# Performance work log

Measured on AMD Instinct MI355X. Metric: run time of the kernel, lower is better.

The kernel has to match this reference:

```python
import jax, jax.numpy as jnp
import numpy as np

N, C, H, W = 8, 256, 28, 28
K = 64
EPS = 1e-12  # F.normalize eps
BN_EPS = 1e-5


def setup_inputs() -> dict:
    key = jax.random.key(0)
    k1, k2, k3 = jax.random.split(key, 3)
    x = jax.random.normal(k1, (N, C, H, W), dtype=jnp.float32)
    conv_w = jax.random.normal(k2, (K, C), dtype=jnp.float32) * 0.05  # 1x1 conv, no bias (vlad_v2=False)
    centroids = jax.random.uniform(k3, (K, C), dtype=jnp.float32)    # torch.rand init
    bn_w = jnp.ones((K * C,), dtype=jnp.float32)
    bn_b = jnp.zeros((K * C,), dtype=jnp.float32)
    return {"x": x, "conv_w": conv_w, "centroids": centroids, "bn_w": bn_w, "bn_b": bn_b}


def _l2norm(v, axis):
    n = jnp.sqrt(jnp.sum(v * v, axis=axis, keepdims=True))
    return v / jnp.maximum(n, EPS)


def reference(x, conv_w, centroids, bn_w, bn_b):
    n, c, h, w = x.shape
    k = centroids.shape[0]
    P = h * w
    # descriptor-wise L2 normalize over channels
    xn = _l2norm(x, axis=1)
    xf = xn.reshape(n, c, P)                                   # (N, C, P)
    # 1x1 conv soft assignment + softmax over clusters
    soft_assign = jnp.einsum('ncp,kc->nkp', xf, conv_w)        # (N, K, P)
    soft_assign = jax.nn.softmax(soft_assign, axis=1)
    # weighted residuals (N, K, C, P)
    residual = (xf[:, None, :, :] - centroids[None, :, :, None]) * soft_assign[:, :, None, :]
    # intra-normalize over flattened (K*C) per spatial location
    rn = jnp.sqrt(jnp.sum(residual * residual, axis=(1, 2), keepdims=True))  # (N,1,1,P)
    residual = residual / jnp.maximum(rn, EPS)
    # sum pool over spatial, then per-cluster L2 normalize over C
    vlad = residual.sum(axis=-1)                               # (N, K, C)
    vlad = _l2norm(vlad, axis=2)
    v = vlad.reshape(n, k * c)
    # BatchNorm1d in training mode: batch stats, biased variance
    mean = jnp.mean(v, axis=0)
    var = jnp.var(v, axis=0)
    v = (v - mean) / jnp.sqrt(var + BN_EPS) * bn_w + bn_b
    # final L2 normalize
    return _l2norm(v, axis=1)
```

## Files before the change

kernel.cpp:

```cpp
#include <hip/hip_runtime.h>
#include <math.h>

#define N_ 8
#define C_ 256
#define P_ 784
#define K_ 64
#define F_ 16384
#define FEPS 1e-12f
#define BNEPS 1e-5f
#define PBLK 25

__device__ __forceinline__ float wave_sum(float v) {
#pragma unroll
  for (int s = 1; s < 64; s <<= 1) v += __shfl_xor(v, s, 64);
  return v;
}
__device__ __forceinline__ float wave_max(float v) {
#pragma unroll
  for (int s = 1; s < 64; s <<= 1) v = fmaxf(v, __shfl_xor(v, s, 64));
  return v;
}

__global__ __launch_bounds__(512) void k_fused1(const float* __restrict__ x,
                                                const float* __restrict__ convw,
                                                const float* __restrict__ cent,
                                                float* __restrict__ w2,
                                                float* __restrict__ Spart) {
  __shared__ float As[128][33];
  __shared__ float Xs[32][34];
  __shared__ float G_lds[128][33];
  __shared__ float w2_lds[64][36];
  __shared__ float cn2p[64][9];
  __shared__ float cn2_lds[64];
  __shared__ float ssq_lds[16][33];
  __shared__ float rinv_lds[32];
  __shared__ float xn2_lds[32];
  __shared__ float sp_lds[8][65];

  int pblk = blockIdx.x, n = blockIdx.y;
  int p0 = pblk * 32;
  int t = threadIdx.x;
  int wv = t >> 6, lane = t & 63;
  const float* xb = x + (size_t)n * C_ * P_;

  {
    int k = t >> 3, oct = t & 7;
    const float* row = cent + (size_t)k * C_ + oct * 32;
    float s = 0.f;
#pragma unroll
    for (int i = 0; i < 8; ++i) {
      float4 v = *(const float4*)&row[i * 4];
      s += v.x * v.x + v.y * v.y + v.z * v.z + v.w * v.w;
    }
    cn2p[k][oct] = s;
  }

  int tx = t & 15, ty = t >> 4;
  int spp = t & 31, scg = t >> 5;
  float acc[4][2] = {};
  float ssq_reg = 0.f;

  for (int ch = 0; ch < 8; ++ch) {
    int c0 = ch * 32;
    {
      int cc = t & 31, kg = t >> 5;
#pragma unroll
      for (int i = 0; i < 8; ++i) {
        int kk = kg * 8 + i;
        const float* Ar = (kk < 64) ? (convw + (size_t)kk * C_) : (cent + (size_t)(kk - 64) * C_);
        As[kk][cc] = Ar[c0 + cc];
      }
    }
    {
      int p = p0 + spp;
      bool ok = p < P_;
#pragma unroll
      for (int i = 0; i < 2; ++i) {
        int cl = scg * 2 + i;
        float v = ok ? xb[(size_t)(c0 + cl) * P_ + p] : 0.f;
        Xs[cl][spp] = v;
        ssq_reg += v * v;
      }
    }
    __syncthreads();
    if (ch == 0 && t < 64) {
      float s = 0.f;
#pragma unroll
      for (int i = 0; i < 8; ++i) s += cn2p[t][i];
      cn2_lds[t] = s;
    }
#pragma unroll
    for (int cc = 0; cc < 32; ++cc) {
      float2 xv = *(const float2*)&Xs[cc][tx * 2];
      float a0 = As[ty * 4 + 0][cc];
      float a1 = As[ty * 4 + 1][cc];
      float a2 = As[ty * 4 + 2][cc];
      float a3 = As[ty * 4 + 3][cc];
      acc[0][0] += a0 * xv.x; acc[0][1] += a0 * xv.y;
      acc[1][0] += a1 * xv.x; acc[1][1] += a1 * xv.y;
      acc[2][0] += a2 * xv.x; acc[2][1] += a2 * xv.y;
      acc[3][0] += a3 * xv.x; acc[3][1] += a3 * xv.y;
    }
    __syncthreads();
  }

#pragma unroll
  for (int i = 0; i < 4; ++i) {
    G_lds[ty * 4 + i][tx * 2 + 0] = acc[i][0];
    G_lds[ty * 4 + i][tx * 2 + 1] = acc[i][1];
  }
  ssq_lds[scg][spp] = ssq_reg;
  __syncthreads();
  if (t < 32) {
    float s = 0.f;
#pragma unroll
    for (int g = 0; g < 16; ++g) s += ssq_lds[g][t];
    float r = 1.0f / fmaxf(sqrtf(s), FEPS);
    rinv_lds[t] = r;
    xn2_lds[t] = s * r * r;
  }
  __syncthreads();

  float s_acc = 0.f;
  float c2 = cn2_lds[lane];
#pragma unroll
  for (int j = 0; j < 4; ++j) {
    int pl = wv * 4 + j;
    if (p0 + pl < P_) {
      float r = rinv_lds[pl];
      float x2 = xn2_lds[pl];
      float lg = G_lds[lane][pl] * r;
      float dt = G_lds[64 + lane][pl] * r;
      float m = wave_max(lg);
      float e = expf(lg - m);
      float ssum = wave_sum(e);
      float a = e / ssum;
      float rn2 = wave_sum(a * a * (x2 - 2.f * dt + c2));
      float wf = 1.0f / fmaxf(sqrtf(rn2), FEPS);
      float wval = a * wf;
      s_acc += wval;
      w2_lds[lane][pl] = wval * r;
    }
  }
  sp_lds[wv][lane] = s_acc;
  __syncthreads();
  if (t < 64) {
    float s = 0.f;
#pragma unroll
    for (int g = 0; g < 8; ++g) s += sp_lds[g][t];
    Spart[((size_t)pblk * N_ + n) * 64 + t] = s;
  }
  {
    int k = t >> 3, q = t & 7;
    int p = p0 + q * 4;
    if (p + 3 < P_) {
      float4 v = *(const float4*)&w2_lds[k][q * 4];
      *(float4*)&w2[((size_t)n * K_ + k) * P_ + p] = v;
    }
  }
}

__global__ __launch_bounds__(256) void k_gemm2(const float* __restrict__ x,
                                               const float* __restrict__ w2,
                                               float* __restrict__ vpart) {
  __shared__ float WsT[32][68];
  __shared__ float XsT[32][68];
  int n = blockIdx.z, s = blockIdx.y;
  int c0 = blockIdx.x * 64;
  int t = threadIdx.x;
  int tx = t & 15, ty = t >> 4;
  float acc[4][4] = {};
  const float* wb = w2 + (size_t)n * K_ * P_;
  const float* xb = x + (size_t)n * C_ * P_;
  int pbase = s * 98;
  for (int q = 0; q < 98; q += 32) {
    int r = t >> 5, pc = t & 31;
    bool ok = (q + pc) < 98;
    int p = pbase + q + pc;
#pragma unroll
    for (int i = 0; i < 8; ++i) {
      int row = r + i * 8;
      WsT[pc][row] = ok ? wb[(size_t)row * P_ + p] : 0.f;
      XsT[pc][row] = ok ? xb[(size_t)(c0 + row) * P_ + p] : 0.f;
    }
    __syncthreads();
#pragma unroll
    for (int pp = 0; pp < 32; ++pp) {
      float4 a = *(const float4*)&WsT[pp][ty * 4];
      float4 bv = *(const float4*)&XsT[pp][tx * 4];
      float av[4] = {a.x, a.y, a.z, a.w};
      float bb[4] = {bv.x, bv.y, bv.z, bv.w};
#pragma unroll
      for (int i = 0; i < 4; ++i)
#pragma unroll
        for (int j = 0; j < 4; ++j) acc[i][j] += av[i] * bb[j];
    }
    __syncthreads();
  }
  float* vb = vpart + (size_t)(s * N_ + n) * K_ * C_;
#pragma unroll
  for (int i = 0; i < 4; ++i)
#pragma unroll
    for (int j = 0; j < 4; ++j)
      vb[(size_t)(ty * 4 + i) * C_ + c0 + tx * 4 + j] = acc[i][j];
}

__global__ __launch_bounds__(256) void k_vladnorm(const float* __restrict__ vpart,
                                                  const float* __restrict__ cent,
                                                  const float* __restrict__ Spart,
                                                  float* __restrict__ vladn) {
  __shared__ float red[4];
  int b = blockIdx.x;
  int n = b >> 6, k = b & 63;
  int c = threadIdx.x;
  float Sb = 0.f;
#pragma unroll
  for (int s = 0; s < PBLK; ++s) Sb += Spart[((size_t)s * N_ + n) * 64 + k];
  float val = 0.f;
#pragma unroll
  for (int s = 0; s < 8; ++s) val += vpart[(size_t)(s * 512 + b) * C_ + c];
  val -= cent[(size_t)k * C_ + c] * Sb;
  float ss = wave_sum(val * val);
  int wv = threadIdx.x >> 6, lane = threadIdx.x & 63;
  if (lane == 0) red[wv] = ss;
  __syncthreads();
  float tot = red[0] + red[1] + red[2] + red[3];
  float inv = 1.0f / fmaxf(sqrtf(tot), FEPS);
  vladn[(size_t)b * C_ + c] = val * inv;
}

__global__ __launch_bounds__(256) void k_bn(const float* __restrict__ vladn,
                                            const float* __restrict__ bnw,
                                            const float* __restrict__ bnb,
                                            float* __restrict__ ybuf,
                                            float* __restrict__ nrmpart) {
  __shared__ float red[4][8];
  int f = blockIdx.x * 256 + threadIdx.x;
  float v[N_];
  float s = 0.f;
#pragma unroll
  for (int n = 0; n < N_; ++n) { v[n] = vladn[(size_t)n * F_ + f]; s += v[n]; }
  float mean = s * (1.0f / N_);
  float s2 = 0.f;
#pragma unroll
  for (int n = 0; n < N_; ++n) { float d = v[n] - mean; s2 += d * d; }
  float var = s2 * (1.0f / N_);
  float sc = bnw[f] / sqrtf(var + BNEPS);
  float bb = bnb[f];
  float y[N_];
#pragma unroll
  for (int n = 0; n < N_; ++n) {
    y[n] = (v[n] - mean) * sc + bb;
    ybuf[(size_t)n * F_ + f] = y[n];
  }
  int wv = threadIdx.x >> 6, lane = threadIdx.x & 63;
#pragma unroll
  for (int n = 0; n < N_; ++n) {
    float q = wave_sum(y[n] * y[n]);
    if (lane == 0) red[wv][n] = q;
  }
  __syncthreads();
  if (threadIdx.x < N_) {
    int n = threadIdx.x;
    nrmpart[n * 64 + blockIdx.x] = red[0][n] + red[1][n] + red[2][n] + red[3][n];
  }
}

__global__ __launch_bounds__(256) void k_final(const float* __restrict__ ybuf,
                                               const float* __restrict__ nrmpart,
                                               float* __restrict__ out) {
  int idx = blockIdx.x * 256 + threadIdx.x;
  int n = idx >> 14;
  float tot = 0.f;
#pragma unroll
  for (int b = 0; b < 64; ++b) tot += nrmpart[n * 64 + b];
  float inv = 1.0f / fmaxf(sqrtf(tot), FEPS);
  out[idx] = ybuf[idx] * inv;
}

extern "C" void kernel_launch(void* const* d_in, const int* in_sizes, int n_in,
                              void* d_out, int out_size, void* d_ws, size_t ws_size,
                              hipStream_t stream) {
  const float* x = (const float*)d_in[0];
  const float* convw = (const float*)d_in[1];
  const float* cent = (const float*)d_in[2];
  const float* bnw = (const float*)d_in[3];
  const float* bnb = (const float*)d_in[4];
  float* out = (float*)d_out;
  float* ws = (float*)d_ws;

  float* Spart = ws;
  float* nrmpart = ws + 12800;
  float* w2 = ws + 13312;
  float* vpart = ws + 414720;
  float* vladn = ws + 1463296;
  float* ybuf = ws + 1594368;

  k_fused1<<<dim3(PBLK, N_), 512, 0, stream>>>(x, convw, cent, w2, Spart);
  k_gemm2<<<dim3(4, 8, 8), 256, 0, stream>>>(x, w2, vpart);
  k_vladnorm<<<512, 256, 0, stream>>>(vpart, cent, Spart, vladn);
  k_bn<<<64, 256, 0, stream>>>(vladn, bnw, bnb, ybuf, nrmpart);
  k_final<<<512, 256, 0, stream>>>(ybuf, nrmpart, out);
}
```

Before: 57.41 us.

## Double-buffer weight tiles and read x directly from global in fused GEMM

The first kernel's channel loop now double-buffers the conv weight and centroid tile in LDS, prefetching the next chunk into registers while computing the current one, so each iteration needs one barrier instead of two. The x tile is no longer staged in LDS; each thread loads its float2 columns straight from global memory, and the per-pixel sum of squares is computed in registers by wave 0 instead of a separate LDS reduction. This cuts LDS traffic and synchronization but relies on cache hits for repeated global x reads across the 32 thread rows that share the same columns. The last pixel block clamps its column pointer, so out-of-range columns read duplicate data that is later masked.

```diff
diff --git a/kernel.cpp b/kernel.cpp
--- a/kernel.cpp
+++ b/kernel.cpp
@@ -26,22 +26,25 @@
                                                 const float* __restrict__ cent,
                                                 float* __restrict__ w2,
                                                 float* __restrict__ Spart) {
-  __shared__ float As[128][33];
-  __shared__ float Xs[32][34];
-  __shared__ float G_lds[128][33];
+  __shared__ float As[2][128][36];
+  __shared__ float G_lds[128][34];
   __shared__ float w2_lds[64][36];
   __shared__ float cn2p[64][9];
   __shared__ float cn2_lds[64];
-  __shared__ float ssq_lds[16][33];
   __shared__ float rinv_lds[32];
   __shared__ float xn2_lds[32];
   __shared__ float sp_lds[8][65];
 
-  int pblk = blockIdx.x, n = blockIdx.y;
-  int p0 = pblk * 32;
-  int t = threadIdx.x;
-  int wv = t >> 6, lane = t & 63;
+  const int pblk = blockIdx.x, n = blockIdx.y;
+  const int p0 = pblk * 32;
+  const int t = threadIdx.x;
+  const int wv = t >> 6, lane = t & 63;
   const float* xb = x + (size_t)n * C_ * P_;
+
+  const int tx = t & 15, ty = t >> 4;
+  const int scc = t & 31, skg = t >> 5;
+  const int pbase = p0 + tx * 2;
+  const float* xcol = xb + ((pbase + 1 < P_) ? pbase : (P_ - 2));
 
   {
     int k = t >> 3, oct = t & 7;
@@ -54,70 +57,83 @@
     }
     cn2p[k][oct] = s;
   }
-
-  int tx = t & 15, ty = t >> 4;
-  int spp = t & 31, scg = t >> 5;
+#pragma unroll
+  for (int i = 0; i < 8; ++i) {
+    int kk = skg * 8 + i;
+    const float* Ar = (kk < 64) ? (convw + (size_t)kk * C_) : (cent + (size_t)(kk - 64) * C_);
+    As[0][kk][scc] = Ar[scc];
+  }
+  __syncthreads();
+  if (t < 64) {
+    float s = 0.f;
+#pragma unroll
+    for (int i = 0; i < 8; ++i) s += cn2p[t][i];
+    cn2_lds[t] = s;
+  }
+
   float acc[4][2] = {};
-  float ssq_reg = 0.f;
+  float ssq0 = 0.f, ssq1 = 0.f;
 
   for (int ch = 0; ch < 8; ++ch) {
-    int c0 = ch * 32;
-    {
-      int cc = t & 31, kg = t >> 5;
+    const int cur = ch & 1;
+    const int c0 = ch * 32;
+    float anext[8];
+    if (ch < 7) {
+      int c0n = c0 + 32;
 #pragma unroll
       for (int i = 0; i < 8; ++i) {
-        int kk = kg * 8 + i;
+        int kk = skg * 8 + i;
         const float* Ar = (kk < 64) ? (convw + (size_t)kk * C_) : (cent + (size_t)(kk - 64) * C_);
-        As[kk][cc] = Ar[c0 + cc];
+        anext[i] = Ar[c0n + scc];
       }
     }
-    {
-      int p = p0 + spp;
-      bool ok = p < P_;
-#pragma unroll
-      for (int i = 0; i < 2; ++i) {
-        int cl = scg * 2 + i;
-        float v = ok ? xb[(size_t)(c0 + cl) * P_ + p] : 0.f;
-        Xs[cl][spp] = v;
-        ssq_reg += v * v;
+    const float* xc = xcol + (size_t)c0 * P_;
+#pragma unroll
+    for (int cc4 = 0; cc4 < 32; cc4 += 4) {
+      float2 xv0 = *(const float2*)&xc[(size_t)(cc4 + 0) * P_];
+      float2 xv1 = *(const float2*)&xc[(size_t)(cc4 + 1) * P_];
+      float2 xv2 = *(const float2*)&xc[(size_t)(cc4 + 2) * P_];
+      float2 xv3 = *(const float2*)&xc[(size_t)(cc4 + 3) * P_];
+      float4 a0 = *(const float4*)&As[cur][ty * 4 + 0][cc4];
+      float4 a1 = *(const float4*)&As[cur][ty * 4 + 1][cc4];
+      float4 a2 = *(const float4*)&As[cur][ty * 4 + 2][cc4];
+      float4 a3 = *(const float4*)&As[cur][ty * 4 + 3][cc4];
+      float xa[4] = {xv0.x, xv1.x, xv2.x, xv3.x};
+      float xbv[4] = {xv0.y, xv1.y, xv2.y, xv3.y};
+      float av[4][4] = {{a0.x, a0.y, a0.z, a0.w},
+                        {a1.x, a1.y, a1.z, a1.w},
+                        {a2.x, a2.y, a2.z, a2.w},
+                        {a3.x, a3.y, a3.z, a3.w}};
+#pragma unroll
+      for (int i = 0; i < 4; ++i)
+#pragma unroll
+        for (int j = 0; j < 4; ++j) {
+          acc[i][0] += av[i][j] * xa[j];
+          acc[i][1] += av[i][j] * xbv[j];
+        }
+      if (wv == 0) {
+#pragma unroll
+        for (int j = 0; j < 4; ++j) { ssq0 += xa[j] * xa[j]; ssq1 += xbv[j] * xbv[j]; }
       }
     }
+    if (ch < 7) {
+      const int nxt = cur ^ 1;
+#pragma unroll
+      for (int i = 0; i < 8; ++i) As[nxt][skg * 8 + i][scc] = anext[i];
+    }
     __syncthreads();
-    if (ch == 0 && t < 64) {
-      float s = 0.f;
-#pragma unroll
-      for (int i = 0; i < 8; ++i) s += cn2p[t][i];
-      cn2_lds[t] = s;
-    }
-#pragma unroll
-    for (int cc = 0; cc < 32; ++cc) {
-      float2 xv = *(const float2*)&Xs[cc][tx * 2];
-      float a0 = As[ty * 4 + 0][cc];
-      float a1 = As[ty * 4 + 1][cc];
-      float a2 = As[ty * 4 + 2][cc];
-      float a3 = As[ty * 4 + 3][cc];
-      acc[0][0] += a0 * xv.x; acc[0][1] += a0 * xv.y;
-      acc[1][0] += a1 * xv.x; acc[1][1] += a1 * xv.y;
-      acc[2][0] += a2 * xv.x; acc[2][1] += a2 * xv.y;
-      acc[3][0] += a3 * xv.x; acc[3][1] += a3 * xv.y;
-    }
-    __syncthreads();
-  }
-
-#pragma unroll
-  for (int i = 0; i < 4; ++i) {
-    G_lds[ty * 4 + i][tx * 2 + 0] = acc[i][0];
-    G_lds[ty * 4 + i][tx * 2 + 1] = acc[i][1];
-  }
-  ssq_lds[scg][spp] = ssq_reg;
-  __syncthreads();
-  if (t < 32) {
-    float s = 0.f;
-#pragma unroll
-    for (int g = 0; g < 16; ++g) s += ssq_lds[g][t];
-    float r = 1.0f / fmaxf(sqrtf(s), FEPS);
-    rinv_lds[t] = r;
-    xn2_lds[t] = s * r * r;
+  }
+
+#pragma unroll
+  for (int i = 0; i < 4; ++i)
+    *(float2*)&G_lds[ty * 4 + i][tx * 2] = make_float2(acc[i][0], acc[i][1]);
+  if (t < 16) {
+    float r0 = 1.0f / fmaxf(sqrtf(ssq0), FEPS);
+    float r1 = 1.0f / fmaxf(sqrtf(ssq1), FEPS);
+    rinv_lds[tx * 2] = r0;
+    rinv_lds[tx * 2 + 1] = r1;
+    xn2_lds[tx * 2] = ssq0 * r0 * r0;
+    xn2_lds[tx * 2 + 1] = ssq1 * r1 * r1;
   }
   __syncthreads();
 
```

Measured after the change: 61.58 us. 1.07x slower.
